# Optimization experiments

Hardware: AMD Instinct MI355X
Metric: run time of the kernel (lower is better)

The kernel has to match this reference:

```python
import jax, jax.numpy as jnp
import numpy as np

N, E, IN, H, C = 50000, 800000, 128, 128, 4


def setup_inputs() -> dict:
    key = jax.random.key(0)
    ks = jax.random.split(key, 16)
    s = 0.05
    x = jax.random.normal(ks[0], (N, IN), jnp.float32)
    edge_index = jax.random.randint(ks[1], (2, E), 0, N, jnp.int32)
    inp = {"x": x, "edge_index": edge_index}
    dims = [(IN, H), (H, H), (H, H)]  # per-layer (fan_in, fan_out)
    for i, (fi, fo) in enumerate(dims):
        inp[f"Wl{i}"] = jax.random.normal(ks[2 + 3 * i], (fo, fi), jnp.float32) * s  # neighbor lin (lin_l)
        inp[f"bl{i}"] = jax.random.normal(ks[3 + 3 * i], (fo,), jnp.float32) * s
        inp[f"Wr{i}"] = jax.random.normal(ks[4 + 3 * i], (fo, fi), jnp.float32) * s  # root lin (lin_r, no bias)
    inp["Wh1"] = jax.random.normal(ks[11], (H // 2, H), jnp.float32) * s
    inp["bh1"] = jax.random.normal(ks[12], (H // 2,), jnp.float32) * s
    inp["Wh2"] = jax.random.normal(ks[13], (C, H // 2), jnp.float32) * s
    inp["bh2"] = jax.random.normal(ks[14], (C,), jnp.float32) * s
    return inp


def _sage(x, src, dst, Wl, bl, Wr):
    # mean aggregation of source features at destination nodes
    deg = jax.ops.segment_sum(jnp.ones((src.shape[0],), x.dtype), dst, num_segments=N)
    agg = jax.ops.segment_sum(x[src], dst, num_segments=N)
    mean = agg / jnp.maximum(deg, 1.0)[:, None]
    return mean @ Wl.T + bl + x @ Wr.T


def reference(x, edge_index, Wl0, bl0, Wr0, Wl1, bl1, Wr1, Wl2, bl2, Wr2, Wh1, bh1, Wh2, bh2):
    src, dst = edge_index[0], edge_index[1]
    h = jax.nn.relu(_sage(x, src, dst, Wl0, bl0, Wr0))
    h = jax.nn.relu(_sage(h, src, dst, Wl1, bl1, Wr1))
    h = jax.nn.relu(_sage(h, src, dst, Wl2, bl2, Wr2))
    # head MLP (dropout is identity in eval)
    h = jax.nn.relu(h @ Wh1.T + bh1)
    return h @ Wh2.T + bh2
```

## Files before the change

### kernel.cpp

```cpp
#include <hip/hip_runtime.h>
#include <cstdint>
#include <cstddef>


typedef __attribute__((ext_vector_type(8))) short short8;
typedef __attribute__((ext_vector_type(8))) unsigned short ushort8;
typedef __attribute__((ext_vector_type(4))) float floatx4;

#define BSHIFT 7
#define MAXB 512

__device__ __forceinline__ float bf2f(unsigned short h) {
    return __uint_as_float(((unsigned int)h) << 16);
}
__device__ __forceinline__ void split2(float x, unsigned short& hi, unsigned short& lo) {
    unsigned int u = __float_as_uint(x);
    hi = (unsigned short)(u >> 16);
    float r = x - __uint_as_float(u & 0xFFFF0000u);
    lo = (unsigned short)(__float_as_uint(r) >> 16);
}


__global__ __launch_bounds__(256) void prep_kernel(
    const float* __restrict__ x, unsigned short* __restrict__ xH, int total4,
    const float* __restrict__ w0, const float* __restrict__ w1,
    const float* __restrict__ w2, const float* __restrict__ w3,
    const float* __restrict__ w4, const float* __restrict__ w5,
    unsigned short* __restrict__ WH, unsigned short* __restrict__ WL,
    const int* __restrict__ dst, int E, int* __restrict__ bh, int NBUCK,
    int XB, int WB, int HB) {
    __shared__ int lh[MAXB];
    int bid = blockIdx.x;
    int tid = threadIdx.x;
    if (bid < XB) {
        int i = bid * 256 + tid;
        if (i < total4) {
            float4 v = ((const float4*)x)[i];
            ushort4 h;
            h.x = (unsigned short)(__float_as_uint(v.x) >> 16);
            h.y = (unsigned short)(__float_as_uint(v.y) >> 16);
            h.z = (unsigned short)(__float_as_uint(v.z) >> 16);
            h.w = (unsigned short)(__float_as_uint(v.w) >> 16);
            ((ushort4*)xH)[i] = h;
        }
    } else if (bid < XB + WB) {
        int wb = bid - XB;
        int m = wb >> 4;
        const float* src = (m == 0) ? w0 : (m == 1) ? w1 : (m == 2) ? w2
                           : (m == 3) ? w3 : (m == 4) ? w4 : w5;
        int i = ((wb & 15) << 8) + tid;
        float4 v = ((const float4*)src)[i];
        unsigned short h0, h1, h2, h3, l0, l1, l2, l3;
        split2(v.x, h0, l0); split2(v.y, h1, l1);
        split2(v.z, h2, l2); split2(v.w, h3, l3);
        ((ushort4*)(WH + (size_t)m * 16384))[i] = make_ushort4(h0, h1, h2, h3);
        ((ushort4*)(WL + (size_t)m * 16384))[i] = make_ushort4(l0, l1, l2, l3);
    } else {
        int hbid = bid - XB - WB;
        for (int i = tid; i < NBUCK; i += 256) lh[i] = 0;
        __syncthreads();
        for (int e = hbid * 256 + tid; e < E; e += HB * 256)
            atomicAdd(&lh[dst[e] >> BSHIFT], 1);
        __syncthreads();
        for (int i = tid; i < NBUCK; i += 256)
            if (lh[i]) atomicAdd(&bh[i], lh[i]);
    }
}


__global__ __launch_bounds__(512) void bucket_scan_kernel(const int* __restrict__ bh,
                                                          int* __restrict__ bucket_base,
                                                          int* __restrict__ bucket_cursor,
                                                          int* __restrict__ row_ptr,
                                                          int NBUCK, int N, int E) {
    __shared__ int s[512];
    int tid = threadIdx.x;
    int v = (tid < NBUCK) ? bh[tid] : 0;
    s[tid] = v;
    __syncthreads();
#pragma unroll
    for (int off = 1; off < 512; off <<= 1) {
        int t = (tid >= off) ? s[tid - off] : 0;
        __syncthreads();
        s[tid] += t;
        __syncthreads();
    }
    int excl = s[tid] - v;
    if (tid < NBUCK) { bucket_base[tid] = excl; bucket_cursor[tid] = excl; }
    if (tid == 0) { bucket_base[NBUCK] = E; row_ptr[N] = E; }
}


__global__ __launch_bounds__(256) void binsort_kernel(const int* __restrict__ src,
                                                      const int* __restrict__ dst,
                                                      int E, int CHUNK,
                                                      int* __restrict__ bucket_cursor,
                                                      unsigned int* __restrict__ ebuf,
                                                      int NBUCK) {
    __shared__ int lh[MAXB];
    __shared__ int lcur[MAXB];
    __shared__ int gbase[MAXB];
    int e0 = blockIdx.x * CHUNK;
    int e1 = e0 + CHUNK; if (e1 > E) e1 = E;
    for (int i = threadIdx.x; i < NBUCK; i += 256) { lh[i] = 0; lcur[i] = 0; }
    __syncthreads();
    for (int e = e0 + threadIdx.x; e < e1; e += 256)
        atomicAdd(&lh[dst[e] >> BSHIFT], 1);
    __syncthreads();
    for (int b = threadIdx.x; b < NBUCK; b += 256) {
        int c = lh[b];
        gbase[b] = c ? atomicAdd(&bucket_cursor[b], c) : 0;
    }
    __syncthreads();
    for (int e = e0 + threadIdx.x; e < e1; e += 256) {
        int d = dst[e];
        int s = src[e];
        int b = d >> BSHIFT;
        int off = atomicAdd(&lcur[b], 1);
        ebuf[gbase[b] + off] = (unsigned int)s | ((unsigned int)d << 16);
    }
}


__global__ __launch_bounds__(256) void bucket_fill_kernel(const int* __restrict__ bucket_base,
                                                          const unsigned int* __restrict__ ebuf,
                                                          int* __restrict__ row_ptr,
                                                          int* __restrict__ col, int N) {
    __shared__ int cnt[256];
    __shared__ int scan[256];
    __shared__ int cur[256];
    int b = blockIdx.x;
    int nbase = b << BSHIFT;
    int tid = threadIdx.x;
    int gB = bucket_base[b];
    int gEnd = bucket_base[b + 1];
    cnt[tid] = 0;
    __syncthreads();
    for (int e = gB + tid; e < gEnd; e += 256)
        atomicAdd(&cnt[(ebuf[e] >> 16) - nbase], 1);
    __syncthreads();
    int v = cnt[tid];
    scan[tid] = v;
    __syncthreads();
#pragma unroll
    for (int off = 1; off < 256; off <<= 1) {
        int t = (tid >= off) ? scan[tid - off] : 0;
        __syncthreads();
        scan[tid] += t;
        __syncthreads();
    }
    int excl = scan[tid] - v;
    int n = nbase + tid;
    if (tid < 128 && n < N) row_ptr[n] = gB + excl;
    cur[tid] = gB + excl;
    __syncthreads();
    for (int e = gB + tid; e < gEnd; e += 256) {
        unsigned int pv = ebuf[e];
        int s = (int)(pv & 0xFFFFu);
        int d = (int)(pv >> 16);
        int p = atomicAdd(&cur[d - nbase], 1);
        col[p] = s;
    }
}


__global__ __launch_bounds__(256) void agg_mean_kernel(
    const unsigned short* __restrict__ inH,
    const int* __restrict__ row_ptr, const int* __restrict__ col,
    unsigned short* __restrict__ mH, int N) {
    int wave = threadIdx.x >> 6;
    int lane = threadIdx.x & 63;
    int n = blockIdx.x * 4 + wave;
    if (n >= N) return;
    int quarter = lane >> 4;
    int li = lane & 15;
    int beg = row_ptr[n];
    int end = row_ptr[n + 1];
    float a0 = 0.f, a1 = 0.f, a2 = 0.f, a3 = 0.f;
    float a4 = 0.f, a5 = 0.f, a6 = 0.f, a7 = 0.f;
    float b0 = 0.f, b1 = 0.f, b2 = 0.f, b3 = 0.f;
    float b4 = 0.f, b5 = 0.f, b6 = 0.f, b7 = 0.f;
    int i = beg + quarter;
    for (; i + 4 < end; i += 8) {
        int s0 = col[i], s1 = col[i + 4];
        ushort8 h0 = ((const ushort8*)(inH + (size_t)s0 * 128))[li];
        ushort8 h1 = ((const ushort8*)(inH + (size_t)s1 * 128))[li];
        a0 += bf2f(h0[0]); a1 += bf2f(h0[1]); a2 += bf2f(h0[2]); a3 += bf2f(h0[3]);
        a4 += bf2f(h0[4]); a5 += bf2f(h0[5]); a6 += bf2f(h0[6]); a7 += bf2f(h0[7]);
        b0 += bf2f(h1[0]); b1 += bf2f(h1[1]); b2 += bf2f(h1[2]); b3 += bf2f(h1[3]);
        b4 += bf2f(h1[4]); b5 += bf2f(h1[5]); b6 += bf2f(h1[6]); b7 += bf2f(h1[7]);
    }
    for (; i < end; i += 4) {
        int s0 = col[i];
        ushort8 h0 = ((const ushort8*)(inH + (size_t)s0 * 128))[li];
        a0 += bf2f(h0[0]); a1 += bf2f(h0[1]); a2 += bf2f(h0[2]); a3 += bf2f(h0[3]);
        a4 += bf2f(h0[4]); a5 += bf2f(h0[5]); a6 += bf2f(h0[6]); a7 += bf2f(h0[7]);
    }
    a0 += b0; a1 += b1; a2 += b2; a3 += b3;
    a4 += b4; a5 += b5; a6 += b6; a7 += b7;
    a0 += __shfl_down(a0, 16); a1 += __shfl_down(a1, 16);
    a2 += __shfl_down(a2, 16); a3 += __shfl_down(a3, 16);
    a4 += __shfl_down(a4, 16); a5 += __shfl_down(a5, 16);
    a6 += __shfl_down(a6, 16); a7 += __shfl_down(a7, 16);
    a0 += __shfl_down(a0, 32); a1 += __shfl_down(a1, 32);
    a2 += __shfl_down(a2, 32); a3 += __shfl_down(a3, 32);
    a4 += __shfl_down(a4, 32); a5 += __shfl_down(a5, 32);
    a6 += __shfl_down(a6, 32); a7 += __shfl_down(a7, 32);
    if (quarter == 0) {
        int d = end - beg;
        float inv = 1.0f / (float)(d > 0 ? d : 1);
        ushort8 o;
        o[0] = (unsigned short)(__float_as_uint(a0 * inv) >> 16);
        o[1] = (unsigned short)(__float_as_uint(a1 * inv) >> 16);
        o[2] = (unsigned short)(__float_as_uint(a2 * inv) >> 16);
        o[3] = (unsigned short)(__float_as_uint(a3 * inv) >> 16);
        o[4] = (unsigned short)(__float_as_uint(a4 * inv) >> 16);
        o[5] = (unsigned short)(__float_as_uint(a5 * inv) >> 16);
        o[6] = (unsigned short)(__float_as_uint(a6 * inv) >> 16);
        o[7] = (unsigned short)(__float_as_uint(a7 * inv) >> 16);
        ((ushort8*)(mH + (size_t)n * 128))[li] = o;
    }
}

__global__ __launch_bounds__(256, 2) void sage_gemm_mfma(
    const unsigned short* __restrict__ a0H, const unsigned short* __restrict__ a1H,
    const unsigned short* __restrict__ wlH, const unsigned short* __restrict__ wlL,
    const unsigned short* __restrict__ wrH, const unsigned short* __restrict__ wrL,
    const float* __restrict__ bias,
    unsigned short* __restrict__ outH, int N) {
    __shared__ unsigned short Ah[128][40];
    __shared__ unsigned short Wh[128][40];
    __shared__ unsigned short Wl[128][40];
    int tid = threadIdx.x;
    int n0 = blockIdx.x * 128;
    int wv = tid >> 6, lane = tid & 63;
    int wm = wv & 1, wn = wv >> 1;
    int r16 = lane & 15, q = lane >> 4, q8 = q * 8;

    floatx4 acc[4][4];
#pragma unroll
    for (int mi = 0; mi < 4; ++mi)
#pragma unroll
        for (int ni = 0; ni < 4; ++ni) {
            floatx4 z = {0.f, 0.f, 0.f, 0.f};
            acc[mi][ni] = z;
        }

    int tc = (tid & 3) * 8;
    int tr = tid >> 2;

    for (int part = 0; part < 2; ++part) {
        const unsigned short* AH = part ? a1H : a0H;
        const unsigned short* WHp = part ? wrH : wlH;
        const unsigned short* WLp = part ? wrL : wlL;
        for (int kk = 0; kk < 128; kk += 32) {
            __syncthreads();
#pragma unroll
            for (int rr = 0; rr < 2; ++rr) {
                int row = tr + 64 * rr;
                int n = n0 + row;
                ushort8 vh = {0, 0, 0, 0, 0, 0, 0, 0};
                if (n < N) vh = *(const ushort8*)&AH[(size_t)n * 128 + kk + tc];
                *(ushort8*)&Ah[row][tc] = vh;
                *(ushort8*)&Wh[row][tc] = *(const ushort8*)&WHp[(size_t)row * 128 + kk + tc];
                *(ushort8*)&Wl[row][tc] = *(const ushort8*)&WLp[(size_t)row * 128 + kk + tc];
            }
            __syncthreads();
            short8 ah[4];
#pragma unroll
            for (int mi = 0; mi < 4; ++mi)
                ah[mi] = *(const short8*)&Ah[64 * wm + 16 * mi + r16][q8];
#pragma unroll
            for (int ni = 0; ni < 4; ++ni) {
                int row = 64 * wn + 16 * ni + r16;
                short8 bh = *(const short8*)&Wh[row][q8];
                short8 bl = *(const short8*)&Wl[row][q8];
#pragma unroll
                for (int mi = 0; mi < 4; ++mi) {
                    acc[mi][ni] = __builtin_amdgcn_mfma_f32_16x16x32_bf16(ah[mi], bh, acc[mi][ni], 0, 0, 0);
                    acc[mi][ni] = __builtin_amdgcn_mfma_f32_16x16x32_bf16(ah[mi], bl, acc[mi][ni], 0, 0, 0);
                }
            }
        }
    }

#pragma unroll
    for (int ni = 0; ni < 4; ++ni) {
        int j = 64 * wn + 16 * ni + r16;
        float b = bias[j];
#pragma unroll
        for (int mi = 0; mi < 4; ++mi) {
            floatx4 v = acc[mi][ni];
#pragma unroll
            for (int p = 0; p < 4; ++p) {
                int node = n0 + 64 * wm + 16 * mi + 4 * q + p;
                if (node < N) {
                    float val = fmaxf(v[p] + b, 0.f);
                    outH[(size_t)node * 128 + j] =
                        (unsigned short)(__float_as_uint(val) >> 16);
                }
            }
        }
    }
}


__global__ __launch_bounds__(256) void head_fused_kernel(
    const unsigned short* __restrict__ hH,
    const float* __restrict__ Wh1, const float* __restrict__ bh1,
    const float* __restrict__ Wh2, const float* __restrict__ bh2,
    float* __restrict__ out, int N) {
    __shared__ float As[64][33];
    __shared__ float Bs[32][65];
    __shared__ float Hs[64][65];
    int tid = threadIdx.x;
    int n0 = blockIdx.x * 64;
    int ti = tid & 15;
    int tj = tid >> 4;

    float acc[4][4];
#pragma unroll
    for (int r = 0; r < 4; ++r)
#pragma unroll
        for (int c = 0; c < 4; ++c) acc[r][c] = 0.f;

    for (int kk = 0; kk < 128; kk += 32) {
        int ks = tid & 31, i0 = tid >> 5;
#pragma unroll
        for (int r = 0; r < 8; ++r) {
            int i = i0 + 8 * r;
            int n = n0 + i;
            As[i][ks] = (n < N) ? bf2f(hH[(size_t)n * 128 + kk + ks]) : 0.f;
        }
        int jj0 = tid >> 5;
#pragma unroll
        for (int r = 0; r < 8; ++r) {
            int j = jj0 + 8 * r;
            Bs[ks][j] = Wh1[(size_t)j * 128 + kk + ks];
        }
        __syncthreads();
#pragma unroll 4
        for (int k = 0; k < 32; ++k) {
            float4 b = *(const float4*)&Bs[k][4 * tj];
#pragma unroll
            for (int r = 0; r < 4; ++r) {
                float a = As[4 * ti + r][k];
                acc[r][0] += a * b.x; acc[r][1] += a * b.y;
                acc[r][2] += a * b.z; acc[r][3] += a * b.w;
            }
        }
        __syncthreads();
    }
    float4 bv = *(const float4*)&bh1[4 * tj];
#pragma unroll
    for (int r = 0; r < 4; ++r) {
        int i = 4 * ti + r;
        Hs[i][4 * tj + 0] = fmaxf(acc[r][0] + bv.x, 0.f);
        Hs[i][4 * tj + 1] = fmaxf(acc[r][1] + bv.y, 0.f);
        Hs[i][4 * tj + 2] = fmaxf(acc[r][2] + bv.z, 0.f);
        Hs[i][4 * tj + 3] = fmaxf(acc[r][3] + bv.w, 0.f);
    }
    __syncthreads();
    int ni = tid >> 2;
    int c = tid & 3;
    const float* w = Wh2 + (size_t)c * 64;
    float s = bh2[c];
#pragma unroll 8
    for (int k = 0; k < 64; ++k) s += Hs[ni][k] * w[k];
    int n = n0 + ni;
    if (n < N) out[(size_t)n * 4 + c] = s;
}


extern "C" void kernel_launch(void* const* d_in, const int* in_sizes, int n_in,
                              void* d_out, int out_size, void* d_ws, size_t ws_size,
                              hipStream_t stream) {
    const float* x   = (const float*)d_in[0];
    const int*   ei  = (const int*)d_in[1];
    const float* Wl0 = (const float*)d_in[2];
    const float* bl0 = (const float*)d_in[3];
    const float* Wr0 = (const float*)d_in[4];
    const float* Wl1 = (const float*)d_in[5];
    const float* bl1 = (const float*)d_in[6];
    const float* Wr1 = (const float*)d_in[7];
    const float* Wl2 = (const float*)d_in[8];
    const float* bl2 = (const float*)d_in[9];
    const float* Wr2 = (const float*)d_in[10];
    const float* Wh1 = (const float*)d_in[11];
    const float* bh1 = (const float*)d_in[12];
    const float* Wh2 = (const float*)d_in[13];
    const float* bh2 = (const float*)d_in[14];
    float* out = (float*)d_out;

    const int N = in_sizes[0] / 128;
    const int E = in_sizes[1] / 2;
    const int* src = ei;
    const int* dst = ei + E;
    const int NBUCK = ((N + 127) >> BSHIFT);

    int* row_ptr       = (int*)d_ws;
    int* bh            = row_ptr + N + 1;
    int* bucket_base   = bh + NBUCK;
    int* bucket_cursor = bucket_base + NBUCK + 1;
    unsigned int* ebuf = (unsigned int*)(bucket_cursor + NBUCK);
    int* col           = (int*)(ebuf + E);
    size_t ioff = (((size_t)(N + 1 + 3 * NBUCK + 1 + 2 * (size_t)E)) * sizeof(int) + 255) & ~(size_t)255;
    unsigned short* u0H = (unsigned short*)((char*)d_ws + ioff);
    unsigned short* mHb = u0H + (size_t)N * 128;
    unsigned short* aH  = mHb + (size_t)N * 128;
    unsigned short* WH  = aH + (size_t)N * 128;
    unsigned short* WL  = WH + 6 * 16384;

    const int nb4 = (N + 3) / 4;
    const int gb64 = (N + 63) / 64;
    const int gb128 = (N + 127) / 128;
    const int CHUNK = 2048;
    const int nchunk = (E + CHUNK - 1) / CHUNK;
    const int XB = (N * 32 + 255) / 256;
    const int WB = 96;
    const int HB = 256;

    hipMemsetAsync(bh, 0, (size_t)NBUCK * sizeof(int), stream);
    prep_kernel<<<XB + WB + HB, 256, 0, stream>>>(x, u0H, N * 32,
                                                  Wl0, Wr0, Wl1, Wr1, Wl2, Wr2,
                                                  WH, WL, dst, E, bh, NBUCK, XB, WB, HB);
    bucket_scan_kernel<<<1, 512, 0, stream>>>(bh, bucket_base, bucket_cursor, row_ptr, NBUCK, N, E);
    binsort_kernel<<<nchunk, 256, 0, stream>>>(src, dst, E, CHUNK, bucket_cursor, ebuf, NBUCK);
    bucket_fill_kernel<<<NBUCK, 256, 0, stream>>>(bucket_base, ebuf, row_ptr, col, N);

    agg_mean_kernel<<<nb4, 256, 0, stream>>>(u0H, row_ptr, col, mHb, N);
    sage_gemm_mfma<<<gb128, 256, 0, stream>>>(mHb, u0H,
                                              WH + 0 * 16384, WL + 0 * 16384,
                                              WH + 1 * 16384, WL + 1 * 16384,
                                              bl0, aH, N);
    agg_mean_kernel<<<nb4, 256, 0, stream>>>(aH, row_ptr, col, mHb, N);
    sage_gemm_mfma<<<gb128, 256, 0, stream>>>(mHb, aH,
                                              WH + 2 * 16384, WL + 2 * 16384,
                                              WH + 3 * 16384, WL + 3 * 16384,
                                              bl1, u0H, N);
    agg_mean_kernel<<<nb4, 256, 0, stream>>>(u0H, row_ptr, col, mHb, N);
    sage_gemm_mfma<<<gb128, 256, 0, stream>>>(mHb, u0H,
                                              WH + 4 * 16384, WL + 4 * 16384,
                                              WH + 5 * 16384, WL + 5 * 16384,
                                              bl2, aH, N);

    head_fused_kernel<<<gb64, 256, 0, stream>>>(aH, Wh1, bh1, Wh2, bh2, out, N);
}
```

Measured before the change: 317.6 us.

## Fuse last SAGE GEMM with head MLP using MFMA for first head layer

Replaces the final SAGE GEMM and separate FP32 head kernel with one fused kernel that keeps the layer-3 activations in shared memory as bf16, runs the first head linear layer with bf16 MFMA (hi/lo split weights prepared in prep_kernel), then computes the 4-class output. This removes the global write and reread of the last hidden layer and one launch, and moves the head GEMM from scalar FP32 onto the matrix cores. It adds shared-memory pressure and a bf16 rounding of the head activations, which changes numerics slightly.

```diff
diff --git a/kernel.cpp b/kernel.cpp
--- a/kernel.cpp
+++ b/kernel.cpp
@@ -26,6 +26,7 @@
     const float* __restrict__ w0, const float* __restrict__ w1,
     const float* __restrict__ w2, const float* __restrict__ w3,
     const float* __restrict__ w4, const float* __restrict__ w5,
+    const float* __restrict__ wh1,
     unsigned short* __restrict__ WH, unsigned short* __restrict__ WL,
     const int* __restrict__ dst, int E, int* __restrict__ bh, int NBUCK,
     int XB, int WB, int HB) {
@@ -45,16 +46,28 @@
         }
     } else if (bid < XB + WB) {
         int wb = bid - XB;
-        int m = wb >> 4;
-        const float* src = (m == 0) ? w0 : (m == 1) ? w1 : (m == 2) ? w2
-                           : (m == 3) ? w3 : (m == 4) ? w4 : w5;
-        int i = ((wb & 15) << 8) + tid;
-        float4 v = ((const float4*)src)[i];
-        unsigned short h0, h1, h2, h3, l0, l1, l2, l3;
-        split2(v.x, h0, l0); split2(v.y, h1, l1);
-        split2(v.z, h2, l2); split2(v.w, h3, l3);
-        ((ushort4*)(WH + (size_t)m * 16384))[i] = make_ushort4(h0, h1, h2, h3);
-        ((ushort4*)(WL + (size_t)m * 16384))[i] = make_ushort4(l0, l1, l2, l3);
+        if (wb < 96) {
+            int m = wb >> 4;
+            const float* src = (m == 0) ? w0 : (m == 1) ? w1 : (m == 2) ? w2
+                               : (m == 3) ? w3 : (m == 4) ? w4 : w5;
+            int i = ((wb & 15) << 8) + tid;
+            float4 v = ((const float4*)src)[i];
+            unsigned short h0, h1, h2, h3, l0, l1, l2, l3;
+            split2(v.x, h0, l0); split2(v.y, h1, l1);
+            split2(v.z, h2, l2); split2(v.w, h3, l3);
+            ((ushort4*)(WH + (size_t)m * 16384))[i] = make_ushort4(h0, h1, h2, h3);
+            ((ushort4*)(WL + (size_t)m * 16384))[i] = make_ushort4(l0, l1, l2, l3);
+        } else {
+            int i = ((wb - 96) << 8) + tid;
+            if (i < 2048) {
+                float4 v = ((const float4*)wh1)[i];
+                unsigned short h0, h1, h2, h3, l0, l1, l2, l3;
+                split2(v.x, h0, l0); split2(v.y, h1, l1);
+                split2(v.z, h2, l2); split2(v.w, h3, l3);
+                ((ushort4*)(WH + (size_t)6 * 16384))[i] = make_ushort4(h0, h1, h2, h3);
+                ((ushort4*)(WL + (size_t)6 * 16384))[i] = make_ushort4(l0, l1, l2, l3);
+            }
+        }
     } else {
         int hbid = bid - XB - WB;
         for (int i = tid; i < NBUCK; i += 256) lh[i] = 0;
@@ -222,6 +235,7 @@
     }
 }
 
+
 __global__ __launch_bounds__(256, 2) void sage_gemm_mfma(
     const unsigned short* __restrict__ a0H, const unsigned short* __restrict__ a1H,
     const unsigned short* __restrict__ wlH, const unsigned short* __restrict__ wlL,
@@ -304,71 +318,153 @@
     }
 }
 
-
-__global__ __launch_bounds__(256) void head_fused_kernel(
-    const unsigned short* __restrict__ hH,
-    const float* __restrict__ Wh1, const float* __restrict__ bh1,
-    const float* __restrict__ Wh2, const float* __restrict__ bh2,
-    float* __restrict__ out, int N) {
-    __shared__ float As[64][33];
-    __shared__ float Bs[32][65];
-    __shared__ float Hs[64][65];
+#define SM_AH 0
+#define SM_WH 5120
+#define SM_WL 10240
+#define SM_HS 0
+#define SM_H1 17408
+
+__global__ __launch_bounds__(256, 2) void sage_gemm_head_fused(
+    const unsigned short* __restrict__ a0H, const unsigned short* __restrict__ a1H,
+    const unsigned short* __restrict__ wlH, const unsigned short* __restrict__ wlL,
+    const unsigned short* __restrict__ wrH, const unsigned short* __restrict__ wrL,
+    const float* __restrict__ bias,
+    const unsigned short* __restrict__ wh1H, const unsigned short* __restrict__ wh1L,
+    const float* __restrict__ bh1, const float* __restrict__ Wh2,
+    const float* __restrict__ bh2, float* __restrict__ out, int N) {
+    __shared__ unsigned short smem[26112];
     int tid = threadIdx.x;
-    int n0 = blockIdx.x * 64;
-    int ti = tid & 15;
-    int tj = tid >> 4;
-
-    float acc[4][4];
-#pragma unroll
-    for (int r = 0; r < 4; ++r)
-#pragma unroll
-        for (int c = 0; c < 4; ++c) acc[r][c] = 0.f;
-
-    for (int kk = 0; kk < 128; kk += 32) {
-        int ks = tid & 31, i0 = tid >> 5;
-#pragma unroll
-        for (int r = 0; r < 8; ++r) {
-            int i = i0 + 8 * r;
-            int n = n0 + i;
-            As[i][ks] = (n < N) ? bf2f(hH[(size_t)n * 128 + kk + ks]) : 0.f;
-        }
-        int jj0 = tid >> 5;
-#pragma unroll
-        for (int r = 0; r < 8; ++r) {
-            int j = jj0 + 8 * r;
-            Bs[ks][j] = Wh1[(size_t)j * 128 + kk + ks];
-        }
-        __syncthreads();
-#pragma unroll 4
-        for (int k = 0; k < 32; ++k) {
-            float4 b = *(const float4*)&Bs[k][4 * tj];
-#pragma unroll
-            for (int r = 0; r < 4; ++r) {
-                float a = As[4 * ti + r][k];
-                acc[r][0] += a * b.x; acc[r][1] += a * b.y;
-                acc[r][2] += a * b.z; acc[r][3] += a * b.w;
-            }
-        }
-        __syncthreads();
-    }
-    float4 bv = *(const float4*)&bh1[4 * tj];
-#pragma unroll
-    for (int r = 0; r < 4; ++r) {
-        int i = 4 * ti + r;
-        Hs[i][4 * tj + 0] = fmaxf(acc[r][0] + bv.x, 0.f);
-        Hs[i][4 * tj + 1] = fmaxf(acc[r][1] + bv.y, 0.f);
-        Hs[i][4 * tj + 2] = fmaxf(acc[r][2] + bv.z, 0.f);
-        Hs[i][4 * tj + 3] = fmaxf(acc[r][3] + bv.w, 0.f);
-    }
-    __syncthreads();
-    int ni = tid >> 2;
-    int c = tid & 3;
-    const float* w = Wh2 + (size_t)c * 64;
-    float s = bh2[c];
-#pragma unroll 8
-    for (int k = 0; k < 64; ++k) s += Hs[ni][k] * w[k];
-    int n = n0 + ni;
-    if (n < N) out[(size_t)n * 4 + c] = s;
+    int n0 = blockIdx.x * 128;
+    int wv = tid >> 6, lane = tid & 63;
+    int wm = wv & 1, wn = wv >> 1;
+    int r16 = lane & 15, q = lane >> 4, q8 = q * 8;
+
+    floatx4 acc[4][4];
+#pragma unroll
+    for (int mi = 0; mi < 4; ++mi)
+#pragma unroll
+        for (int ni = 0; ni < 4; ++ni) {
+            floatx4 z = {0.f, 0.f, 0.f, 0.f};
+            acc[mi][ni] = z;
+        }
+
+    int tc = (tid & 3) * 8;
+    int tr = tid >> 2;
+
+    for (int part = 0; part < 2; ++part) {
+        const unsigned short* AH = part ? a1H : a0H;
+        const unsigned short* WHp = part ? wrH : wlH;
+        const unsigned short* WLp = part ? wrL : wlL;
+        for (int kk = 0; kk < 128; kk += 32) {
+            __syncthreads();
+#pragma unroll
+            for (int rr = 0; rr < 2; ++rr) {
+                int row = tr + 64 * rr;
+                int n = n0 + row;
+                ushort8 vh = {0, 0, 0, 0, 0, 0, 0, 0};
+                if (n < N) vh = *(const ushort8*)&AH[(size_t)n * 128 + kk + tc];
+                *(ushort8*)&smem[SM_AH + row * 40 + tc] = vh;
+                *(ushort8*)&smem[SM_WH + row * 40 + tc] = *(const ushort8*)&WHp[(size_t)row * 128 + kk + tc];
+                *(ushort8*)&smem[SM_WL + row * 40 + tc] = *(const ushort8*)&WLp[(size_t)row * 128 + kk + tc];
+            }
+            __syncthreads();
+            short8 ah[4];
+#pragma unroll
+            for (int mi = 0; mi < 4; ++mi)
+                ah[mi] = *(const short8*)&smem[SM_AH + (64 * wm + 16 * mi + r16) * 40 + q8];
+#pragma unroll
+            for (int ni = 0; ni < 4; ++ni) {
+                int row = 64 * wn + 16 * ni + r16;
+                short8 bh = *(const short8*)&smem[SM_WH + row * 40 + q8];
+                short8 bl = *(const short8*)&smem[SM_WL + row * 40 + q8];
+#pragma unroll
+                for (int mi = 0; mi < 4; ++mi) {
+                    acc[mi][ni] = __builtin_amdgcn_mfma_f32_16x16x32_bf16(ah[mi], bh, acc[mi][ni], 0, 0, 0);
+                    acc[mi][ni] = __builtin_amdgcn_mfma_f32_16x16x32_bf16(ah[mi], bl, acc[mi][ni], 0, 0, 0);
+                }
+            }
+        }
+    }
+
+    __syncthreads();
+#pragma unroll
+    for (int ni = 0; ni < 4; ++ni) {
+        int j = 64 * wn + 16 * ni + r16;
+        float b = bias[j];
+#pragma unroll
+        for (int mi = 0; mi < 4; ++mi) {
+            floatx4 v = acc[mi][ni];
+#pragma unroll
+            for (int p = 0; p < 4; ++p) {
+                int row = 64 * wm + 16 * mi + 4 * q + p;
+                float val = fmaxf(v[p] + b, 0.f);
+                smem[SM_HS + row * 136 + j] = (unsigned short)(__float_as_uint(val) >> 16);
+            }
+        }
+    }
+    __syncthreads();
+
+    floatx4 acc2[2][4];
+#pragma unroll
+    for (int t = 0; t < 2; ++t)
+#pragma unroll
+        for (int nt = 0; nt < 4; ++nt) {
+            floatx4 z = {0.f, 0.f, 0.f, 0.f};
+            acc2[t][nt] = z;
+        }
+#pragma unroll
+    for (int ks = 0; ks < 4; ++ks) {
+        short8 at[2];
+#pragma unroll
+        for (int t = 0; t < 2; ++t)
+            at[t] = *(const short8*)&smem[SM_HS + (16 * (2 * wv + t) + r16) * 136 + 32 * ks + q8];
+#pragma unroll
+        for (int nt = 0; nt < 4; ++nt) {
+            int jrow = 16 * nt + r16;
+            short8 bh = *(const short8*)&wh1H[jrow * 128 + 32 * ks + q8];
+            short8 bl = *(const short8*)&wh1L[jrow * 128 + 32 * ks + q8];
+#pragma unroll
+            for (int t = 0; t < 2; ++t) {
+                acc2[t][nt] = __builtin_amdgcn_mfma_f32_16x16x32_bf16(at[t], bh, acc2[t][nt], 0, 0, 0);
+                acc2[t][nt] = __builtin_amdgcn_mfma_f32_16x16x32_bf16(at[t], bl, acc2[t][nt], 0, 0, 0);
+            }
+        }
+    }
+#pragma unroll
+    for (int nt = 0; nt < 4; ++nt) {
+        int c = 16 * nt + r16;
+        float b1 = bh1[c];
+#pragma unroll
+        for (int t = 0; t < 2; ++t) {
+            floatx4 v = acc2[t][nt];
+#pragma unroll
+            for (int p = 0; p < 4; ++p) {
+                int row = 16 * (2 * wv + t) + 4 * q + p;
+                float val = fmaxf(v[p] + b1, 0.f);
+                smem[SM_H1 + row * 68 + c] = (unsigned short)(__float_as_uint(val) >> 16);
+            }
+        }
+    }
+    __syncthreads();
+
+    {
+        int row = tid >> 1;
+        int c0 = (tid & 1) * 2;
+        int n = n0 + row;
+        if (n < N) {
+            const float* w0p = Wh2 + (size_t)c0 * 64;
+            const float* w1p = w0p + 64;
+            float s0 = bh2[c0], s1 = bh2[c0 + 1];
+#pragma unroll 16
+            for (int k = 0; k < 64; ++k) {
+                float hv = bf2f(smem[SM_H1 + row * 68 + k]);
+                s0 += hv * w0p[k];
+                s1 += hv * w1p[k];
+            }
+            out[(size_t)n * 4 + c0] = s0;
+            out[(size_t)n * 4 + c0 + 1] = s1;
+        }
+    }
 }
 
 
@@ -409,20 +505,19 @@
     unsigned short* mHb = u0H + (size_t)N * 128;
     unsigned short* aH  = mHb + (size_t)N * 128;
     unsigned short* WH  = aH + (size_t)N * 128;
-    unsigned short* WL  = WH + 6 * 16384;
+    unsigned short* WL  = WH + 6 * 16384 + 8192;
 
     const int nb4 = (N + 3) / 4;
-    const int gb64 = (N + 63) / 64;
     const int gb128 = (N + 127) / 128;
     const int CHUNK = 2048;
     const int nchunk = (E + CHUNK - 1) / CHUNK;
     const int XB = (N * 32 + 255) / 256;
-    const int WB = 96;
+    const int WB = 104;
     const int HB = 256;
 
     hipMemsetAsync(bh, 0, (size_t)NBUCK * sizeof(int), stream);
     prep_kernel<<<XB + WB + HB, 256, 0, stream>>>(x, u0H, N * 32,
-                                                  Wl0, Wr0, Wl1, Wr1, Wl2, Wr2,
+                                                  Wl0, Wr0, Wl1, Wr1, Wl2, Wr2, Wh1,
                                                   WH, WL, dst, E, bh, NBUCK, XB, WB, HB);
     bucket_scan_kernel<<<1, 512, 0, stream>>>(bh, bucket_base, bucket_cursor, row_ptr, NBUCK, N, E);
     binsort_kernel<<<nchunk, 256, 0, stream>>>(src, dst, E, CHUNK, bucket_cursor, ebuf, NBUCK);
@@ -439,10 +534,10 @@
                                               WH + 3 * 16384, WL + 3 * 16384,
                                               bl1, u0H, N);
     agg_mean_kernel<<<nb4, 256, 0, stream>>>(u0H, row_ptr, col, mHb, N);
-    sage_gemm_mfma<<<gb128, 256, 0, stream>>>(mHb, u0H,
-                                              WH + 4 * 16384, WL + 4 * 16384,
-                                              WH + 5 * 16384, WL + 5 * 16384,
-                                              bl2, aH, N);
-
-    head_fused_kernel<<<gb64, 256, 0, stream>>>(aH, Wh1, bh1, Wh2, bh2, out, N);
-}
+    sage_gemm_head_fused<<<gb128, 256, 0, stream>>>(mHb, u0H,
+                                                    WH + 4 * 16384, WL + 4 * 16384,
+                                                    WH + 5 * 16384, WL + 5 * 16384,
+                                                    bl2,
+                                                    WH + 6 * 16384, WL + 6 * 16384,
+                                                    bh1, Wh2, bh2, out, N);
+}
```

After: 293.0 us. 7.7% less time.
